# Kernel optimization log

Hardware: AMD Instinct MI355X
Metric: run time of the kernel (lower is better)

Reference implementation:

```python
import jax, jax.numpy as jnp
import numpy as np

N_POINTS = 100000
N_EVENTS = 1000000
N_PAIRS = 100000      # node_pair_samples
N_RIEMANN = 128       # riemann_samples
INIT_BETA = 0.025
NON_EVENT_W = 1.0
EPS = 1e-6            # torch PairwiseDistance default eps (added to the difference)


def setup_inputs() -> dict:
    key = jax.random.key(0)
    ks = jax.random.split(key, 8)
    # learned parameters
    beta = jnp.full((1, 1), INIT_BETA, jnp.float32)
    z0 = jax.random.uniform(ks[0], (N_POINTS, 2), jnp.float32, -0.025, 0.025)
    v0 = jax.random.uniform(ks[1], (N_POINTS, 2), jnp.float32, -0.025, 0.025)
    a0 = jnp.zeros((N_POINTS, 2), jnp.float32)  # a0 is referenced by step(); zero -> constant-velocity
    # event data: (u, v, event_time)
    u = jax.random.randint(ks[2], (N_EVENTS,), 0, N_POINTS)
    v = jax.random.randint(ks[3], (N_EVENTS,), 0, N_POINTS)
    event_times = jax.random.uniform(ks[4], (N_EVENTS,), jnp.float32, 0.0, 1.0)
    # sampled non-event node pairs (stand-in for randperm over triu indices)
    pair_u = jax.random.randint(ks[5], (N_PAIRS,), 0, N_POINTS)
    pair_v = jax.random.randint(ks[6], (N_PAIRS,), 0, N_POINTS)
    pair_v = jnp.where(pair_v == pair_u, (pair_v + 1) % N_POINTS, pair_v)
    t0 = jnp.float32(0.0)
    tn = jnp.float32(1.0)
    return {"beta": beta, "z0": z0, "v0": v0, "a0": a0,
            "u": u, "v": v, "event_times": event_times,
            "pair_u": pair_u, "pair_v": pair_v, "t0": t0, "tn": tn}


def reference(beta, z0, v0, a0, u, v, event_times, pair_u, pair_v, t0, tn):
    b = beta[0, 0]
    # ---- event intensity: sum_e (beta - ||z_u(t_e) - z_v(t_e)||) ----
    te = event_times[:, None]                                  # [E,1]
    zu = z0[u] + v0[u] * te + 0.5 * a0[u] * te ** 2            # [E,2]
    zv = z0[v] + v0[v] * te + 0.5 * a0[v] * te ** 2            # [E,2]
    d_ev = jnp.sqrt(jnp.sum((zu - zv + EPS) ** 2, axis=-1))    # [E]
    event_intensity = b * event_times.shape[0] - jnp.sum(d_ev)
    # ---- non-event intensity: Riemann sum of exp(beta - d(t)) over sampled pairs ----
    ts = t0 + (jnp.arange(N_RIEMANN, dtype=jnp.float32) / N_RIEMANN) * (tn - t0)  # [T] left Riemann
    dt = (tn - t0) / N_RIEMANN
    dz = z0[pair_u] - z0[pair_v]                               # [P,2]
    dv = v0[pair_u] - v0[pair_v]
    da = a0[pair_u] - a0[pair_v]
    tt = ts[None, :, None]                                     # [1,T,1]
    diff = dz[:, None, :] + dv[:, None, :] * tt + 0.5 * da[:, None, :] * tt ** 2 + EPS  # [P,T,2]
    d_ne = jnp.sqrt(jnp.sum(diff ** 2, axis=-1))               # [P,T]
    non_event_intensity = jnp.sum(jnp.exp(b - d_ne)) * dt
    return event_intensity - NON_EVENT_W * non_event_intensity
```

## Files before the change

kernel.cpp:

```cpp
#include <hip/hip_runtime.h>
#include <hip/hip_fp16.h>

#define N_POINTS   100000
#define N_EVENTS   1000000
#define N_PAIRS    100000
#define N_RIEMANN  128
#define EPS_F      1e-6f
#define NON_EVENT_W 1.0f

constexpr int BLOCK       = 256;
constexpr int EVPT        = 4;
constexpr int EV_THREADS  = N_EVENTS / EVPT;
constexpr int EV_BLOCKS   = (EV_THREADS + BLOCK - 1) / BLOCK;
constexpr int PAIR_BLOCKS = (N_PAIRS + BLOCK - 1) / BLOCK;
constexpr int MAIN_BLOCKS = PAIR_BLOCKS + EV_BLOCKS;
constexpr int PREP_BLOCKS = (N_POINTS + BLOCK - 1) / BLOCK;


__device__ __forceinline__ float block_reduce_sum(float v) {
    #pragma unroll
    for (int off = 32; off > 0; off >>= 1)
        v += __shfl_down(v, off, 64);
    __shared__ float smem[BLOCK / 64];
    const int lane = threadIdx.x & 63;
    const int wid  = threadIdx.x >> 6;
    if (lane == 0) smem[wid] = v;
    __syncthreads();
    float r = 0.f;
    if (threadIdx.x == 0) {
        #pragma unroll
        for (int i = 0; i < BLOCK / 64; ++i) r += smem[i];
    }
    return r;
}

__device__ __forceinline__ void decode_rec(const float4& r, float2& z, float2& v, float2& a) {
    z = __half22float2(*reinterpret_cast<const __half2*>(&r.x));
    v = __half22float2(*reinterpret_cast<const __half2*>(&r.y));
    a = __half22float2(*reinterpret_cast<const __half2*>(&r.z));
}

__global__ __launch_bounds__(BLOCK) void prep_kernel(
    const float2* __restrict__ z0,
    const float2* __restrict__ v0,
    const float2* __restrict__ a0,
    const float*  __restrict__ beta,
    float4*       __restrict__ pts,
    float*        __restrict__ out)
{
    const int i = blockIdx.x * BLOCK + threadIdx.x;
    if (i < N_POINTS) {
        const float2 z = z0[i], v = v0[i], a = a0[i];
        float4 r;
        *reinterpret_cast<__half2*>(&r.x) = __float22half2_rn(make_float2(z.x, z.y));
        *reinterpret_cast<__half2*>(&r.y) = __float22half2_rn(make_float2(v.x, v.y));
        *reinterpret_cast<__half2*>(&r.z) = __float22half2_rn(make_float2(a.x, a.y));
        r.w = 0.f;
        pts[i] = r;
    }
    if (blockIdx.x == 0 && threadIdx.x == 0)
        out[0] = beta[0] * (float)N_EVENTS;
}

template <bool PACKED>
__global__ __launch_bounds__(BLOCK) void main_kernel(
    const float4* __restrict__ pts,
    const float2* __restrict__ z0,
    const float2* __restrict__ v0,
    const float2* __restrict__ a0,
    const float*  __restrict__ beta,
    const int*    __restrict__ eu,
    const int*    __restrict__ ev,
    const float*  __restrict__ et,
    const int*    __restrict__ pu,
    const int*    __restrict__ pv,
    const float*  __restrict__ t0p,
    const float*  __restrict__ tnp,
    float*        __restrict__ out)
{
    float acc = 0.f;
    const int b = blockIdx.x;

    if (b < PAIR_BLOCKS) {
        const int p = b * BLOCK + threadIdx.x;
        if (p < N_PAIRS) {
            const float t0v = t0p[0];
            const float tnv = tnp[0];
            const float dt  = (tnv - t0v) * (1.0f / N_RIEMANN);
            const float bb  = beta[0];
            const int iu = pu[p];
            const int iv = pv[p];
            float dzx, dzy, dvx, dvy, dax, day;
            if (PACKED) {
                const float4 ru = pts[iu];
                const float4 rv = pts[iv];
                float2 zu, vu, au, zv, vv, av;
                decode_rec(ru, zu, vu, au);
                decode_rec(rv, zv, vv, av);
                dzx = zu.x - zv.x; dzy = zu.y - zv.y;
                dvx = vu.x - vv.x; dvy = vu.y - vv.y;
                dax = au.x - av.x; day = au.y - av.y;
            } else {
                const float2 zu = z0[iu], zv = z0[iv];
                const float2 vu = v0[iu], vv = v0[iv];
                const float2 au = a0[iu], av = a0[iv];
                dzx = zu.x - zv.x; dzy = zu.y - zv.y;
                dvx = vu.x - vv.x; dvy = vu.y - vv.y;
                dax = au.x - av.x; day = au.y - av.y;
            }
            const float eb = __expf(bb);
            float s = 0.f;
            #pragma unroll 4
            for (int k = 0; k < N_RIEMANN; ++k) {
                const float t = t0v + (float)k * (1.0f / N_RIEMANN) * (tnv - t0v);
                const float h = 0.5f * t * t;
                const float dx = dzx + dvx * t + dax * h + EPS_F;
                const float dy = dzy + dvy * t + day * h + EPS_F;
                s += __expf(-sqrtf(dx * dx + dy * dy));
            }
            acc = -NON_EVENT_W * dt * eb * s;
        }
    } else {
        const int t = (b - PAIR_BLOCKS) * BLOCK + threadIdx.x;
        if (t < EV_THREADS) {
            int iu[EVPT], iv[EVPT];
            float te[EVPT];
            #pragma unroll
            for (int j = 0; j < EVPT; ++j) {
                const int i = t + j * EV_THREADS;
                iu[j] = eu[i];
                iv[j] = ev[i];
                te[j] = et[i];
            }
            if (PACKED) {
                float4 ru[EVPT], rv[EVPT];
                #pragma unroll
                for (int j = 0; j < EVPT; ++j) ru[j] = pts[iu[j]];
                #pragma unroll
                for (int j = 0; j < EVPT; ++j) rv[j] = pts[iv[j]];
                #pragma unroll
                for (int j = 0; j < EVPT; ++j) {
                    float2 zu, vu, au, zv, vv, av;
                    decode_rec(ru[j], zu, vu, au);
                    decode_rec(rv[j], zv, vv, av);
                    const float h = 0.5f * te[j] * te[j];
                    const float dx = (zu.x - zv.x) + (vu.x - vv.x) * te[j] + (au.x - av.x) * h + EPS_F;
                    const float dy = (zu.y - zv.y) + (vu.y - vv.y) * te[j] + (au.y - av.y) * h + EPS_F;
                    acc -= sqrtf(dx * dx + dy * dy);
                }
            } else {
                float2 zu[EVPT], zv[EVPT], vu[EVPT], vv[EVPT], au[EVPT], av[EVPT];
                #pragma unroll
                for (int j = 0; j < EVPT; ++j) { zu[j] = z0[iu[j]]; zv[j] = z0[iv[j]]; }
                #pragma unroll
                for (int j = 0; j < EVPT; ++j) { vu[j] = v0[iu[j]]; vv[j] = v0[iv[j]]; }
                #pragma unroll
                for (int j = 0; j < EVPT; ++j) { au[j] = a0[iu[j]]; av[j] = a0[iv[j]]; }
                #pragma unroll
                for (int j = 0; j < EVPT; ++j) {
                    const float h = 0.5f * te[j] * te[j];
                    const float dx = (zu[j].x - zv[j].x) + (vu[j].x - vv[j].x) * te[j] + (au[j].x - av[j].x) * h + EPS_F;
                    const float dy = (zu[j].y - zv[j].y) + (vu[j].y - vv[j].y) * te[j] + (au[j].y - av[j].y) * h + EPS_F;
                    acc -= sqrtf(dx * dx + dy * dy);
                }
            }
        }
    }

    const float r = block_reduce_sum(acc);
    if (threadIdx.x == 0) atomicAdd(out, r);
}

extern "C" void kernel_launch(void* const* d_in, const int* in_sizes, int n_in,
                              void* d_out, int out_size, void* d_ws, size_t ws_size,
                              hipStream_t stream) {
    const float*  beta = (const float*)d_in[0];
    const float2* z0   = (const float2*)d_in[1];
    const float2* v0   = (const float2*)d_in[2];
    const float2* a0   = (const float2*)d_in[3];
    const int*    eu   = (const int*)d_in[4];
    const int*    ev   = (const int*)d_in[5];
    const float*  et   = (const float*)d_in[6];
    const int*    pu   = (const int*)d_in[7];
    const int*    pv   = (const int*)d_in[8];
    const float*  t0p  = (const float*)d_in[9];
    const float*  tnp  = (const float*)d_in[10];

    float*  out = (float*)d_out;
    float4* pts = (float4*)d_ws;
    const bool packed = (ws_size >= (size_t)N_POINTS * sizeof(float4));

    if (packed) {
        prep_kernel<<<PREP_BLOCKS, BLOCK, 0, stream>>>(z0, v0, a0, beta, pts, out);
        main_kernel<true><<<MAIN_BLOCKS, BLOCK, 0, stream>>>(
            pts, z0, v0, a0, beta, eu, ev, et, pu, pv, t0p, tnp, out);
    } else {
        prep_kernel<<<1, BLOCK, 0, stream>>>(z0, v0, a0, beta, pts, out);
        main_kernel<false><<<MAIN_BLOCKS, BLOCK, 0, stream>>>(
            pts, z0, v0, a0, beta, eu, ev, et, pu, pv, t0p, tnp, out);
    }
}
```

Measured before the change: 109.6 us.

## Vectorize event index loads, double events per thread, replace atomics with partials reduce

Each event thread now handles 8 contiguous events and loads the u, v and time arrays with 128-bit int4/float4 loads instead of strided scalar loads. The per-block atomicAdd onto the output is replaced by writing block partials to workspace, summed by a new single-block reduce kernel that also adds the beta*N term. This aims to cut load instruction count and atomic contention, at the cost of an extra kernel launch, fewer threads for latency hiding, and more registers per thread. The fallback path now needs workspace for partials.

```diff
diff --git a/kernel.cpp b/kernel.cpp
--- a/kernel.cpp
+++ b/kernel.cpp
@@ -9,7 +9,7 @@
 #define NON_EVENT_W 1.0f
 
 constexpr int BLOCK       = 256;
-constexpr int EVPT        = 4;
+constexpr int EVPT        = 8;
 constexpr int EV_THREADS  = N_EVENTS / EVPT;
 constexpr int EV_BLOCKS   = (EV_THREADS + BLOCK - 1) / BLOCK;
 constexpr int PAIR_BLOCKS = (N_PAIRS + BLOCK - 1) / BLOCK;
@@ -44,9 +44,7 @@
     const float2* __restrict__ z0,
     const float2* __restrict__ v0,
     const float2* __restrict__ a0,
-    const float*  __restrict__ beta,
-    float4*       __restrict__ pts,
-    float*        __restrict__ out)
+    float4*       __restrict__ pts)
 {
     const int i = blockIdx.x * BLOCK + threadIdx.x;
     if (i < N_POINTS) {
@@ -58,8 +56,6 @@
         r.w = 0.f;
         pts[i] = r;
     }
-    if (blockIdx.x == 0 && threadIdx.x == 0)
-        out[0] = beta[0] * (float)N_EVENTS;
 }
 
 template <bool PACKED>
@@ -76,7 +72,7 @@
     const int*    __restrict__ pv,
     const float*  __restrict__ t0p,
     const float*  __restrict__ tnp,
-    float*        __restrict__ out)
+    float*        __restrict__ partials)
 {
     float acc = 0.f;
     const int b = blockIdx.x;
@@ -123,15 +119,15 @@
     } else {
         const int t = (b - PAIR_BLOCKS) * BLOCK + threadIdx.x;
         if (t < EV_THREADS) {
-            int iu[EVPT], iv[EVPT];
-            float te[EVPT];
-            #pragma unroll
-            for (int j = 0; j < EVPT; ++j) {
-                const int i = t + j * EV_THREADS;
-                iu[j] = eu[i];
-                iv[j] = ev[i];
-                te[j] = et[i];
-            }
+            const int4*   eu4 = reinterpret_cast<const int4*>(eu);
+            const int4*   ev4 = reinterpret_cast<const int4*>(ev);
+            const float4* et4 = reinterpret_cast<const float4*>(et);
+            const int4 u0 = eu4[2 * t], u1 = eu4[2 * t + 1];
+            const int4 w0 = ev4[2 * t], w1 = ev4[2 * t + 1];
+            const float4 t0q = et4[2 * t], t1q = et4[2 * t + 1];
+            const int iu[EVPT] = { u0.x, u0.y, u0.z, u0.w, u1.x, u1.y, u1.z, u1.w };
+            const int iv[EVPT] = { w0.x, w0.y, w0.z, w0.w, w1.x, w1.y, w1.z, w1.w };
+            const float te[EVPT] = { t0q.x, t0q.y, t0q.z, t0q.w, t1q.x, t1q.y, t1q.z, t1q.w };
             if (PACKED) {
                 float4 ru[EVPT], rv[EVPT];
                 #pragma unroll
@@ -149,18 +145,14 @@
                     acc -= sqrtf(dx * dx + dy * dy);
                 }
             } else {
-                float2 zu[EVPT], zv[EVPT], vu[EVPT], vv[EVPT], au[EVPT], av[EVPT];
-                #pragma unroll
-                for (int j = 0; j < EVPT; ++j) { zu[j] = z0[iu[j]]; zv[j] = z0[iv[j]]; }
-                #pragma unroll
-                for (int j = 0; j < EVPT; ++j) { vu[j] = v0[iu[j]]; vv[j] = v0[iv[j]]; }
-                #pragma unroll
-                for (int j = 0; j < EVPT; ++j) { au[j] = a0[iu[j]]; av[j] = a0[iv[j]]; }
                 #pragma unroll
                 for (int j = 0; j < EVPT; ++j) {
+                    const float2 zu = z0[iu[j]], zv = z0[iv[j]];
+                    const float2 vu = v0[iu[j]], vv = v0[iv[j]];
+                    const float2 au = a0[iu[j]], av = a0[iv[j]];
                     const float h = 0.5f * te[j] * te[j];
-                    const float dx = (zu[j].x - zv[j].x) + (vu[j].x - vv[j].x) * te[j] + (au[j].x - av[j].x) * h + EPS_F;
-                    const float dy = (zu[j].y - zv[j].y) + (vu[j].y - vv[j].y) * te[j] + (au[j].y - av[j].y) * h + EPS_F;
+                    const float dx = (zu.x - zv.x) + (vu.x - vv.x) * te[j] + (au.x - av.x) * h + EPS_F;
+                    const float dy = (zu.y - zv.y) + (vu.y - vv.y) * te[j] + (au.y - av.y) * h + EPS_F;
                     acc -= sqrtf(dx * dx + dy * dy);
                 }
             }
@@ -168,7 +160,18 @@
     }
 
     const float r = block_reduce_sum(acc);
-    if (threadIdx.x == 0) atomicAdd(out, r);
+    if (threadIdx.x == 0) partials[blockIdx.x] = r;
+}
+
+__global__ __launch_bounds__(BLOCK) void reduce_kernel(
+    const float* __restrict__ partials,
+    const float* __restrict__ beta,
+    float*       __restrict__ out)
+{
+    float acc = 0.f;
+    for (int i = threadIdx.x; i < MAIN_BLOCKS; i += BLOCK) acc += partials[i];
+    const float r = block_reduce_sum(acc);
+    if (threadIdx.x == 0) out[0] = beta[0] * (float)N_EVENTS + r;
 }
 
 extern "C" void kernel_launch(void* const* d_in, const int* in_sizes, int n_in,
@@ -186,17 +189,21 @@
     const float*  t0p  = (const float*)d_in[9];
     const float*  tnp  = (const float*)d_in[10];
 
-    float*  out = (float*)d_out;
-    float4* pts = (float4*)d_ws;
-    const bool packed = (ws_size >= (size_t)N_POINTS * sizeof(float4));
+    float* out = (float*)d_out;
+    const size_t pts_bytes = (size_t)N_POINTS * sizeof(float4);
+    const bool packed = (ws_size >= pts_bytes + (size_t)MAIN_BLOCKS * sizeof(float));
 
     if (packed) {
-        prep_kernel<<<PREP_BLOCKS, BLOCK, 0, stream>>>(z0, v0, a0, beta, pts, out);
+        float4* pts      = (float4*)d_ws;
+        float*  partials = (float*)((char*)d_ws + pts_bytes);
+        prep_kernel<<<PREP_BLOCKS, BLOCK, 0, stream>>>(z0, v0, a0, pts);
         main_kernel<true><<<MAIN_BLOCKS, BLOCK, 0, stream>>>(
-            pts, z0, v0, a0, beta, eu, ev, et, pu, pv, t0p, tnp, out);
+            pts, z0, v0, a0, beta, eu, ev, et, pu, pv, t0p, tnp, partials);
+        reduce_kernel<<<1, BLOCK, 0, stream>>>(partials, beta, out);
     } else {
-        prep_kernel<<<1, BLOCK, 0, stream>>>(z0, v0, a0, beta, pts, out);
+        float* partials = (float*)d_ws;
         main_kernel<false><<<MAIN_BLOCKS, BLOCK, 0, stream>>>(
-            pts, z0, v0, a0, beta, eu, ev, et, pu, pv, t0p, tnp, out);
-    }
-}
+            nullptr, z0, v0, a0, beta, eu, ev, et, pu, pv, t0p, tnp, partials);
+        reduce_kernel<<<1, BLOCK, 0, stream>>>(partials, beta, out);
+    }
+}
```

Measured after the change: 105.3 us. -3.9%, faster.
